# Performance work log

Hardware: AMD Instinct MI355X
Metric: run time of the kernel (lower is better)

The kernel has to match this reference:

```python
import jax, jax.numpy as jnp
import numpy as np

B, C, H, W = 16, 256, 56, 56
G, K, R = 16, 3, 2
CR = C // R          # reduced channels = 128
KKG = K * K * G      # span output channels = 144
EPS = 1e-5


def setup_inputs() -> dict:
    key = jax.random.key(0)
    ks = jax.random.split(key, 5)
    return {
        "x": jax.random.normal(ks[0], (B, C, H, W), jnp.float32),
        "w_reduce": jax.random.normal(ks[1], (CR, C), jnp.float32) * 0.05,
        "b_reduce": jax.random.normal(ks[2], (CR,), jnp.float32) * 0.05,
        "gamma": jnp.ones((CR,), jnp.float32),
        "beta": jnp.zeros((CR,), jnp.float32),
        "w_span": jax.random.normal(ks[3], (KKG, CR), jnp.float32) * 0.05,
        "b_span": jax.random.normal(ks[4], (KKG,), jnp.float32) * 0.05,
    }


def _conv1x1(x, w, bias):
    # 1x1 conv == channel contraction
    return jnp.einsum('bchw,oc->bohw', x, w) + bias[None, :, None, None]


def _involution(x, w_reduce, b_reduce, gamma, beta, w_span, b_span):
    b, c, h, w = x.shape
    # kernel-generation branch: reduce -> BN (batch stats) -> ReLU -> span
    t = _conv1x1(x, w_reduce, b_reduce)
    mu = t.mean(axis=(0, 2, 3), keepdims=True)
    var = t.var(axis=(0, 2, 3), keepdims=True)  # biased, as torch BN training
    t = (t - mu) * jax.lax.rsqrt(var + EPS)
    t = t * gamma[None, :, None, None] + beta[None, :, None, None]
    t = jax.nn.relu(t)
    kern = _conv1x1(t, w_span, b_span)  # [b, k*k*g, h, w]
    # 'b (k j g) h w -> b g (k j) h w'
    kern = kern.reshape(b, K, K, G, h, w).transpose(0, 3, 1, 2, 4, 5)
    kern = kern.reshape(b, G, K * K, h, w)
    # unfold x into [b, g, d, k*k, h, w] via shifted padded slices (no dense im2col buffer write pattern beyond necessity)
    p = K // 2
    xp = jnp.pad(x, ((0, 0), (0, 0), (p, p), (p, p)))
    patches = jnp.stack(
        [xp[:, :, i:i + h, j:j + w] for i in range(K) for j in range(K)],
        axis=2)  # [b, c, k*k, h, w]
    patches = patches.reshape(b, G, c // G, K * K, h, w)
    out = jnp.einsum('bgdxhw,bgxhw->bgdhw', patches, kern)  # weighted window sum
    return out.reshape(b, c, h, w)


def reference(x, w_reduce, b_reduce, gamma, beta, w_span, b_span):
    return _involution(x, w_reduce, b_reduce, gamma, beta, w_span, b_span)
```

## Files before the change

### kernel.cpp

```cpp
#include <hip/hip_runtime.h>
#include <hip/hip_bf16.h>

#define B_   16
#define C_   256
#define HW_  3136
#define W_   56
#define CR_  128
#define KKG_ 144
#define G_   16
#define NPOS (B_*HW_)
#define EPS_ 1e-5f
#define NBLK1 1568
#define NBLK3 784

typedef float f32x4 __attribute__((ext_vector_type(4)));
typedef short s16x8 __attribute__((ext_vector_type(8)));
typedef short s16x4 __attribute__((ext_vector_type(4)));

#define T2_OFF_B    0
#define KERN_OFF_B  12845056
#define GACC_OFF_B  27295744
#define WBFR_OFF_B  27296768
#define WBFS_OFF_B  27362304

__device__ inline unsigned short f2bf(float f) {
    unsigned u = __float_as_uint(f);
    u += 0x7fff + ((u >> 16) & 1);
    return (unsigned short)(u >> 16);
}
__device__ inline float bf2f(unsigned short h) {
    return __uint_as_float(((unsigned)h) << 16);
}
__device__ inline unsigned pkcvt(float a, float b) {
    float2 f2; f2.x = a; f2.y = b;
    __hip_bfloat162 h = __float22bfloat162_rn(f2);
    union { __hip_bfloat162 h2; unsigned u; } cv; cv.h2 = h;
    return cv.u;
}

typedef const __attribute__((address_space(1))) unsigned int* gas_t;
typedef __attribute__((address_space(3))) unsigned int* las_t;
__device__ inline void gload_lds16(const void* g, void* l) {
    __builtin_amdgcn_global_load_lds((gas_t)g, (las_t)l, 16, 0, 0);
}
__device__ inline void barrier_raw() {
    __builtin_amdgcn_sched_barrier(0);
    __builtin_amdgcn_s_barrier();
    __builtin_amdgcn_sched_barrier(0);
}

__global__ __launch_bounds__(256) void prep_cast(
    const float* __restrict__ w_reduce, const float* __restrict__ w_span,
    unsigned short* __restrict__ wbfr, unsigned short* __restrict__ wbfs,
    float* __restrict__ gacc)
{
    int idx = blockIdx.x * 256 + threadIdx.x;
    if (idx < 256) gacc[idx] = 0.0f;
    if (idx < 32768) {
        wbfr[idx] = f2bf(w_reduce[idx]);
    } else {
        int k = idx - 32768;
        if (k < 18432) wbfs[k] = f2bf(w_span[k]);
    }
}

__global__ __launch_bounds__(256, 4) void reduce_mfma(
    const float* __restrict__ x, const unsigned short* __restrict__ wbfr,
    unsigned short* __restrict__ t2, float* __restrict__ gacc)
{
    __shared__ __align__(16) float xb3[3][1024];
    __shared__ __align__(16) short awb[3][4096];
    __shared__ float redp[128][2], redq[128][2];

    const int tid = threadIdx.x;
    const int lane = tid & 63, wv = tid >> 6;
    const int q = lane >> 4, i = lane & 15;
    const int q8 = q * 8;
    const int mrow = (wv & 1) * 64;
    const int pw = (wv >> 1) * 16;
    const int blk = blockIdx.x;
    const int b = blk / 98;
    const int p0 = (blk % 98) * 32;

    const int c_st = tid >> 3;
    const int swz = ((tid & 7) ^ ((c_st >> 1) & 7)) * 4;
    const float* xlane = x + (size_t)b * C_ * HW_ + (size_t)c_st * HW_ + p0 + swz;
    const unsigned short* wA0 = wbfr + (size_t)(tid >> 2) * C_ + (tid & 3) * 8;
    const unsigned short* wA1 = wA0 + (size_t)64 * C_;
    const int wvu4 = (tid & ~63) * 4;
    const int wvu8 = (tid & ~63) * 8;

    #define STAGE1(ch, bi) do {                                          \
        gload_lds16(xlane + (size_t)(ch) * 32 * HW_, &xb3[bi][wvu4]);    \
        gload_lds16(wA0 + (ch) * 32, &awb[bi][wvu8]);                    \
        gload_lds16(wA1 + (ch) * 32, &awb[bi][2048 + wvu8]);             \
    } while (0)

    const int p_loc = pw + i;
    const int pg = p_loc >> 2, pe = p_loc & 3;

    f32x4 acc[4] = {};

    STAGE1(0, 0);
    STAGE1(1, 1);

    #pragma unroll
    for (int ch = 0; ch < 8; ch++) {
        const int cur = ch % 3;
        if (ch < 7) asm volatile("s_waitcnt vmcnt(3)" ::: "memory");
        else        asm volatile("s_waitcnt vmcnt(0)" ::: "memory");
        barrier_raw();
        if (ch == 0) STAGE1(2, 2);
        if (ch == 1) STAGE1(3, 0);
        if (ch == 2) STAGE1(4, 1);
        if (ch == 3) STAGE1(5, 2);
        if (ch == 4) STAGE1(6, 0);
        if (ch == 5) STAGE1(7, 1);

        s16x8 af[4];
        #pragma unroll
        for (int mt = 0; mt < 4; mt++)
            af[mt] = *(const s16x8*)&awb[cur][(mrow + mt * 16 + i) * 32 + q8];
        float f[8];
        #pragma unroll
        for (int k = 0; k < 8; k++) {
            int cl = q8 + k;
            int slot = pg ^ ((cl >> 1) & 7);
            f[k] = xb3[cur][cl * 32 + slot * 4 + pe];
        }
        union { s16x8 v; unsigned u[4]; } Bv;
        #pragma unroll
        for (int k2 = 0; k2 < 4; k2++) Bv.u[k2] = pkcvt(f[2*k2], f[2*k2+1]);

        #pragma unroll
        for (int mt = 0; mt < 4; mt++)
            acc[mt] = __builtin_amdgcn_mfma_f32_16x16x32_bf16(
                af[mt], Bv.v, acc[mt], 0, 0, 0);
    }
    #undef STAGE1

    const int p = p0 + pw + i;
    #pragma unroll
    for (int mt = 0; mt < 4; mt++) {
        uint2 pr;
        pr.x = pkcvt(acc[mt][0], acc[mt][1]);
        pr.y = pkcvt(acc[mt][2], acc[mt][3]);
        *(uint2*)(t2 + ((size_t)b * HW_ + p) * CR_ + mrow + mt * 16 + q * 4) = pr;
        #pragma unroll
        for (int reg = 0; reg < 4; reg++) {
            float v = acc[mt][reg];
            float s = v, ss = v * v;
            #pragma unroll
            for (int m = 1; m < 16; m <<= 1) {
                s  += __shfl_xor(s, m);
                ss += __shfl_xor(ss, m);
            }
            if (i == 0) {
                int o = mrow + mt * 16 + q * 4 + reg;
                redp[o][wv >> 1] = s;
                redq[o][wv >> 1] = ss;
            }
        }
    }
    __syncthreads();
    if (tid < 128) atomicAdd(&gacc[tid], redp[tid][0] + redp[tid][1]);
    else           atomicAdd(&gacc[tid], redq[tid - 128][0] + redq[tid - 128][1]);
}

__global__ __launch_bounds__(256, 3) void span_mfma(
    const unsigned short* __restrict__ t2, const unsigned short* __restrict__ wbfs,
    const float* __restrict__ b_span, const float* __restrict__ gacc,
    const float* __restrict__ gamma, const float* __restrict__ beta,
    unsigned short* __restrict__ kern)
{
    __shared__ __align__(16) short aw[144 * 128];
    __shared__ __align__(16) short bb3[3][2048];
    __shared__ float scs[128], shs[128], bsp[144];

    const int tid = threadIdx.x;
    const int lane = tid & 63, wv = tid >> 6;
    const int q = lane >> 4, i = lane & 15;
    const int q8 = q * 8;
    const int blk = blockIdx.x;
    const int b = blk / 49;
    const int p0 = (blk % 49) * 64;

    if (tid < 128) {
        float s = gacc[tid], ss = gacc[128 + tid];
        const float inv_n = 1.0f / (float)NPOS;
        float mu = s * inv_n;
        float var = ss * inv_n - mu * mu;
        float sc = gamma[tid] * rsqrtf(var + EPS_);
        scs[tid] = sc;
        shs[tid] = beta[tid] - mu * sc;
    }
    if (tid < 144) bsp[tid] = b_span[tid];
    __syncthreads();

    const unsigned short* tlane =
        t2 + ((size_t)b * HW_ + p0 + (tid >> 2)) * CR_ + (tid & 3) * 8;
    const int wvu8 = (tid & ~63) * 8;

    #pragma unroll
    for (int e = 0; e < 9; e++) {
        int U = tid + e * 256;
        int r = U >> 4, u = U & 15;
        gload_lds16(wbfs + (size_t)r * CR_ + ((u ^ (r & 7)) * 8),
                    &aw[((tid & ~63) + e * 256) * 8]);
    }
    gload_lds16(tlane,      &bb3[0][wvu8]);
    gload_lds16(tlane + 32, &bb3[1][wvu8]);

    f32x4 acc[9] = {};

    #pragma unroll
    for (int ch = 0; ch < 4; ch++) {
        const int cur = ch % 3;
        if (ch < 3) asm volatile("s_waitcnt vmcnt(1)" ::: "memory");
        else        asm volatile("s_waitcnt vmcnt(0)" ::: "memory");
        barrier_raw();
        if (ch == 0) gload_lds16(tlane + 64, &bb3[2][wvu8]);
        if (ch == 1) gload_lds16(tlane + 96, &bb3[0][wvu8]);

        s16x8 raw = *(const s16x8*)&bb3[cur][(wv * 16 + i) * 32 + q8];
        const int cb = ch * 32 + q8;
        float f[8];
        #pragma unroll
        for (int k = 0; k < 8; k++)
            f[k] = fmaxf(fmaf(bf2f((unsigned short)raw[k]),
                              scs[cb + k], shs[cb + k]), 0.0f);
        union { s16x8 v; unsigned u[4]; } Bv;
        #pragma unroll
        for (int k2 = 0; k2 < 4; k2++) Bv.u[k2] = pkcvt(f[2*k2], f[2*k2+1]);

        #pragma unroll
        for (int mt = 0; mt < 9; mt++) {
            int r = mt * 16 + i;
            int slot = (ch * 4 + q) ^ (r & 7);
            s16x8 af = *(const s16x8*)&aw[r * 128 + slot * 8];
            acc[mt] = __builtin_amdgcn_mfma_f32_16x16x32_bf16(
                af, Bv.v, acc[mt], 0, 0, 0);
        }
    }

    const int p = p0 + wv * 16 + i;
    #pragma unroll
    for (int mt = 0; mt < 9; mt++) {
        #pragma unroll
        for (int reg = 0; reg < 4; reg++) {
            int o2 = mt * 16 + q * 4 + reg;
            int row = (o2 & 15) * 9 + (o2 >> 4);
            kern[((size_t)b * KKG_ + row) * HW_ + p] = f2bf(acc[mt][reg] + bsp[o2]);
        }
    }
}

__global__ __launch_bounds__(256) void involution_apply(
    const float* __restrict__ x, const unsigned short* __restrict__ kern,
    float* __restrict__ out)
{
    const int gtid = blockIdx.x * 256 + threadIdx.x;
    const int pu  = gtid % 784;
    const int bg  = gtid / 784;
    const int g = bg & 15;
    const int b = bg >> 4;
    const int pix0 = pu * 4;
    const int h = pix0 / W_;
    const int w0 = pix0 % W_;

    const unsigned short* kb = kern + ((size_t)(b * G_ + g) * 9) * HW_ + pix0;
    float kvf[9][4];
    #pragma unroll
    for (int kk = 0; kk < 9; kk++) {
        s16x4 kraw = *(const s16x4*)(kb + (size_t)kk * HW_);
        #pragma unroll
        for (int j = 0; j < 4; j++)
            kvf[kk][j] = bf2f((unsigned short)kraw[j]);
    }

    const float* xg = x + (size_t)(b * C_ + g * 16) * HW_;
    float* og = out + (size_t)(b * C_ + g * 16) * HW_ + pix0;

    const bool has_l = (w0 > 0);
    const bool has_r = (w0 + 4 < W_);
    const int loff = has_l ? (w0 - 1) : w0;
    const int roff = has_r ? (w0 + 4) : w0;

    #pragma unroll
    for (int d = 0; d < 16; d++) {
        f32x4 acc = {0.0f, 0.0f, 0.0f, 0.0f};
        const float* xd = xg + (size_t)d * HW_;
        #pragma unroll
        for (int di = 0; di < 3; di++) {
            const int hh = h + di - 1;
            if (hh < 0 || hh >= W_) continue;
            const float* xr = xd + hh * W_;
            float4 mid = *(const float4*)(xr + w0);
            float lv = xr[loff];
            float rv = xr[roff];
            float win[6];
            win[0] = has_l ? lv : 0.0f;
            win[1] = mid.x; win[2] = mid.y; win[3] = mid.z; win[4] = mid.w;
            win[5] = has_r ? rv : 0.0f;
            #pragma unroll
            for (int dj = 0; dj < 3; dj++) {
                #pragma unroll
                for (int j = 0; j < 4; j++)
                    acc[j] = fmaf(win[dj + j], kvf[di * 3 + dj][j], acc[j]);
            }
        }
        *(f32x4*)(og + (size_t)d * HW_) = acc;
    }
}

extern "C" void kernel_launch(void* const* d_in, const int* in_sizes, int n_in,
                              void* d_out, int out_size, void* d_ws, size_t ws_size,
                              hipStream_t stream) {
    const float* x        = (const float*)d_in[0];
    const float* w_reduce = (const float*)d_in[1];
    const float* gamma    = (const float*)d_in[3];
    const float* beta     = (const float*)d_in[4];
    const float* w_span   = (const float*)d_in[5];
    const float* b_span   = (const float*)d_in[6];
    float* out = (float*)d_out;

    char* wsb = (char*)d_ws;
    unsigned short* t2   = (unsigned short*)(wsb + T2_OFF_B);
    unsigned short* kern = (unsigned short*)(wsb + KERN_OFF_B);
    float*          gacc = (float*)(wsb + GACC_OFF_B);
    unsigned short* wbfr = (unsigned short*)(wsb + WBFR_OFF_B);
    unsigned short* wbfs = (unsigned short*)(wsb + WBFS_OFF_B);

    prep_cast<<<200, 256, 0, stream>>>(w_reduce, w_span, wbfr, wbfs, gacc);
    reduce_mfma<<<NBLK1, 256, 0, stream>>>(x, wbfr, t2, gacc);
    span_mfma<<<NBLK3, 256, 0, stream>>>(t2, wbfs, b_span, gacc, gamma, beta, kern);
    involution_apply<<<(B_ * G_ * HW_ / 4) / 256, 256, 0, stream>>>(x, kern, out);
}
```

Measured before the change: 198.8 us.

## Double reduce-kernel position tile and replace BN atomics with per-block partials

The reduce GEMM kernel now handles 64 positions per block instead of 32, halving the grid to 784 blocks. Each wave computes two N-tiles, so each A-fragment load is reused twice, and the x staging buffer doubles with an adjusted swizzle. The BN sum and sum-of-squares atomics are replaced by per-block partial writes. A new bn_finalize kernel reduces those partials and produces scale and shift, which removes atomic contention but adds one kernel launch. Occupancy drops from 4 to 3 blocks per CU because of the larger shared memory footprint.

```diff
diff --git a/kernel.cpp b/kernel.cpp
--- a/kernel.cpp
+++ b/kernel.cpp
@@ -10,8 +10,7 @@
 #define G_   16
 #define NPOS (B_*HW_)
 #define EPS_ 1e-5f
-#define NBLK1 1568
-#define NBLK3 784
+#define NBLK 784
 
 typedef float f32x4 __attribute__((ext_vector_type(4)));
 typedef short s16x8 __attribute__((ext_vector_type(8)));
@@ -19,9 +18,10 @@
 
 #define T2_OFF_B    0
 #define KERN_OFF_B  12845056
-#define GACC_OFF_B  27295744
-#define WBFR_OFF_B  27296768
-#define WBFS_OFF_B  27362304
+#define GP_OFF_B    27295744
+#define STAT_OFF_B  28098560
+#define WBFR_OFF_B  28099584
+#define WBFS_OFF_B  28165120
 
 __device__ inline unsigned short f2bf(float f) {
     unsigned u = __float_as_uint(f);
@@ -51,11 +51,9 @@
 
 __global__ __launch_bounds__(256) void prep_cast(
     const float* __restrict__ w_reduce, const float* __restrict__ w_span,
-    unsigned short* __restrict__ wbfr, unsigned short* __restrict__ wbfs,
-    float* __restrict__ gacc)
+    unsigned short* __restrict__ wbfr, unsigned short* __restrict__ wbfs)
 {
     int idx = blockIdx.x * 256 + threadIdx.x;
-    if (idx < 256) gacc[idx] = 0.0f;
     if (idx < 32768) {
         wbfr[idx] = f2bf(w_reduce[idx]);
     } else {
@@ -64,11 +62,11 @@
     }
 }
 
-__global__ __launch_bounds__(256, 4) void reduce_mfma(
+__global__ __launch_bounds__(256, 3) void reduce_mfma(
     const float* __restrict__ x, const unsigned short* __restrict__ wbfr,
-    unsigned short* __restrict__ t2, float* __restrict__ gacc)
-{
-    __shared__ __align__(16) float xb3[3][1024];
+    unsigned short* __restrict__ t2, float* __restrict__ gp)
+{
+    __shared__ __align__(16) float xb3[3][2048];
     __shared__ __align__(16) short awb[3][4096];
     __shared__ float redp[128][2], redq[128][2];
 
@@ -77,29 +75,30 @@
     const int q = lane >> 4, i = lane & 15;
     const int q8 = q * 8;
     const int mrow = (wv & 1) * 64;
-    const int pw = (wv >> 1) * 16;
+    const int pw = (wv >> 1) * 32;
     const int blk = blockIdx.x;
-    const int b = blk / 98;
-    const int p0 = (blk % 98) * 32;
-
-    const int c_st = tid >> 3;
-    const int swz = ((tid & 7) ^ ((c_st >> 1) & 7)) * 4;
-    const float* xlane = x + (size_t)b * C_ * HW_ + (size_t)c_st * HW_ + p0 + swz;
+    const int b = blk / 49;
+    const int p0 = (blk % 49) * 64;
+
+    const int ce0 = tid >> 4, slot = tid & 15;
+    const int ce1 = ce0 + 16;
+    const float* xs0 = x + (size_t)b * C_ * HW_ + (size_t)ce0 * HW_ + p0
+                         + ((slot ^ ((ce0 >> 2) & 7)) << 2);
+    const float* xs1 = x + (size_t)b * C_ * HW_ + (size_t)ce1 * HW_ + p0
+                         + ((slot ^ ((ce1 >> 2) & 7)) << 2);
     const unsigned short* wA0 = wbfr + (size_t)(tid >> 2) * C_ + (tid & 3) * 8;
     const unsigned short* wA1 = wA0 + (size_t)64 * C_;
     const int wvu4 = (tid & ~63) * 4;
     const int wvu8 = (tid & ~63) * 8;
 
-    #define STAGE1(ch, bi) do {                                          \
-        gload_lds16(xlane + (size_t)(ch) * 32 * HW_, &xb3[bi][wvu4]);    \
-        gload_lds16(wA0 + (ch) * 32, &awb[bi][wvu8]);                    \
-        gload_lds16(wA1 + (ch) * 32, &awb[bi][2048 + wvu8]);             \
+    #define STAGE1(ch, bi) do {                                            \
+        gload_lds16(xs0 + (size_t)(ch) * 32 * HW_, &xb3[bi][wvu4]);        \
+        gload_lds16(xs1 + (size_t)(ch) * 32 * HW_, &xb3[bi][1024 + wvu4]); \
+        gload_lds16(wA0 + (ch) * 32, &awb[bi][wvu8]);                      \
+        gload_lds16(wA1 + (ch) * 32, &awb[bi][2048 + wvu8]);               \
     } while (0)
 
-    const int p_loc = pw + i;
-    const int pg = p_loc >> 2, pe = p_loc & 3;
-
-    f32x4 acc[4] = {};
+    f32x4 acc[4][2] = {};
 
     STAGE1(0, 0);
     STAGE1(1, 1);
@@ -107,7 +106,7 @@
     #pragma unroll
     for (int ch = 0; ch < 8; ch++) {
         const int cur = ch % 3;
-        if (ch < 7) asm volatile("s_waitcnt vmcnt(3)" ::: "memory");
+        if (ch < 7) asm volatile("s_waitcnt vmcnt(4)" ::: "memory");
         else        asm volatile("s_waitcnt vmcnt(0)" ::: "memory");
         barrier_raw();
         if (ch == 0) STAGE1(2, 2);
@@ -121,35 +120,48 @@
         #pragma unroll
         for (int mt = 0; mt < 4; mt++)
             af[mt] = *(const s16x8*)&awb[cur][(mrow + mt * 16 + i) * 32 + q8];
-        float f[8];
-        #pragma unroll
-        for (int k = 0; k < 8; k++) {
-            int cl = q8 + k;
-            int slot = pg ^ ((cl >> 1) & 7);
-            f[k] = xb3[cur][cl * 32 + slot * 4 + pe];
-        }
-        union { s16x8 v; unsigned u[4]; } Bv;
-        #pragma unroll
-        for (int k2 = 0; k2 < 4; k2++) Bv.u[k2] = pkcvt(f[2*k2], f[2*k2+1]);
+
+        s16x8 bfr[2];
+        #pragma unroll
+        for (int nt = 0; nt < 2; nt++) {
+            const int p_loc = pw + nt * 16 + i;
+            const int pg = p_loc >> 2, pe = p_loc & 3;
+            float f[8];
+            #pragma unroll
+            for (int k = 0; k < 8; k++) {
+                int cl = q8 + k;
+                f[k] = xb3[cur][cl * 64 + ((pg ^ ((cl >> 2) & 7)) << 2) + pe];
+            }
+            union { s16x8 v; unsigned u[4]; } Bv;
+            #pragma unroll
+            for (int k2 = 0; k2 < 4; k2++) Bv.u[k2] = pkcvt(f[2*k2], f[2*k2+1]);
+            bfr[nt] = Bv.v;
+        }
 
         #pragma unroll
         for (int mt = 0; mt < 4; mt++)
-            acc[mt] = __builtin_amdgcn_mfma_f32_16x16x32_bf16(
-                af[mt], Bv.v, acc[mt], 0, 0, 0);
+            #pragma unroll
+            for (int nt = 0; nt < 2; nt++)
+                acc[mt][nt] = __builtin_amdgcn_mfma_f32_16x16x32_bf16(
+                    af[mt], bfr[nt], acc[mt][nt], 0, 0, 0);
     }
     #undef STAGE1
 
-    const int p = p0 + pw + i;
     #pragma unroll
     for (int mt = 0; mt < 4; mt++) {
-        uint2 pr;
-        pr.x = pkcvt(acc[mt][0], acc[mt][1]);
-        pr.y = pkcvt(acc[mt][2], acc[mt][3]);
-        *(uint2*)(t2 + ((size_t)b * HW_ + p) * CR_ + mrow + mt * 16 + q * 4) = pr;
+        #pragma unroll
+        for (int nt = 0; nt < 2; nt++) {
+            int p = p0 + pw + nt * 16 + i;
+            uint2 pr;
+            pr.x = pkcvt(acc[mt][nt][0], acc[mt][nt][1]);
+            pr.y = pkcvt(acc[mt][nt][2], acc[mt][nt][3]);
+            *(uint2*)(t2 + ((size_t)b * HW_ + p) * CR_ + mrow + mt * 16 + q * 4) = pr;
+        }
         #pragma unroll
         for (int reg = 0; reg < 4; reg++) {
-            float v = acc[mt][reg];
-            float s = v, ss = v * v;
+            float v0 = acc[mt][0][reg], v1 = acc[mt][1][reg];
+            float s = v0 + v1;
+            float ss = v0 * v0 + v1 * v1;
             #pragma unroll
             for (int m = 1; m < 16; m <<= 1) {
                 s  += __shfl_xor(s, m);
@@ -163,14 +175,46 @@
         }
     }
     __syncthreads();
-    if (tid < 128) atomicAdd(&gacc[tid], redp[tid][0] + redp[tid][1]);
-    else           atomicAdd(&gacc[tid], redq[tid - 128][0] + redq[tid - 128][1]);
+    if (tid < 128)
+        gp[(size_t)tid * NBLK + blk] = redp[tid][0] + redp[tid][1];
+    else
+        gp[(size_t)tid * NBLK + blk] = redq[tid - 128][0] + redq[tid - 128][1];
+}
+
+__global__ __launch_bounds__(256) void bn_finalize(
+    const float* __restrict__ gp, const float* __restrict__ gamma,
+    const float* __restrict__ beta, float* __restrict__ stats)
+{
+    const int o = blockIdx.x;
+    const int tid = threadIdx.x;
+    float s = 0.f, ss = 0.f;
+    for (int idx = tid; idx < NBLK; idx += 256) {
+        s  += gp[(size_t)o * NBLK + idx];
+        ss += gp[(size_t)(128 + o) * NBLK + idx];
+    }
+    #pragma unroll
+    for (int m = 1; m < 64; m <<= 1) {
+        s  += __shfl_xor(s, m);
+        ss += __shfl_xor(ss, m);
+    }
+    __shared__ float rs[4], rss[4];
+    if ((tid & 63) == 0) { rs[tid >> 6] = s; rss[tid >> 6] = ss; }
+    __syncthreads();
+    if (tid == 0) {
+        s  = rs[0] + rs[1] + rs[2] + rs[3];
+        ss = rss[0] + rss[1] + rss[2] + rss[3];
+        float inv_n = 1.0f / (float)NPOS;
+        float mu = s * inv_n;
+        float var = ss * inv_n - mu * mu;
+        float sc = gamma[o] * rsqrtf(var + EPS_);
+        stats[o] = sc;
+        stats[128 + o] = beta[o] - mu * sc;
+    }
 }
 
 __global__ __launch_bounds__(256, 3) void span_mfma(
     const unsigned short* __restrict__ t2, const unsigned short* __restrict__ wbfs,
-    const float* __restrict__ b_span, const float* __restrict__ gacc,
-    const float* __restrict__ gamma, const float* __restrict__ beta,
+    const float* __restrict__ b_span, const float* __restrict__ stats,
     unsigned short* __restrict__ kern)
 {
     __shared__ __align__(16) short aw[144 * 128];
@@ -185,15 +229,7 @@
     const int b = blk / 49;
     const int p0 = (blk % 49) * 64;
 
-    if (tid < 128) {
-        float s = gacc[tid], ss = gacc[128 + tid];
-        const float inv_n = 1.0f / (float)NPOS;
-        float mu = s * inv_n;
-        float var = ss * inv_n - mu * mu;
-        float sc = gamma[tid] * rsqrtf(var + EPS_);
-        scs[tid] = sc;
-        shs[tid] = beta[tid] - mu * sc;
-    }
+    if (tid < 128) { scs[tid] = stats[tid]; shs[tid] = stats[128 + tid]; }
     if (tid < 144) bsp[tid] = b_span[tid];
     __syncthreads();
 
@@ -327,12 +363,14 @@
     char* wsb = (char*)d_ws;
     unsigned short* t2   = (unsigned short*)(wsb + T2_OFF_B);
     unsigned short* kern = (unsigned short*)(wsb + KERN_OFF_B);
-    float*          gacc = (float*)(wsb + GACC_OFF_B);
+    float*          gp    = (float*)(wsb + GP_OFF_B);
+    float*          stats = (float*)(wsb + STAT_OFF_B);
     unsigned short* wbfr = (unsigned short*)(wsb + WBFR_OFF_B);
     unsigned short* wbfs = (unsigned short*)(wsb + WBFS_OFF_B);
 
-    prep_cast<<<200, 256, 0, stream>>>(w_reduce, w_span, wbfr, wbfs, gacc);
-    reduce_mfma<<<NBLK1, 256, 0, stream>>>(x, wbfr, t2, gacc);
-    span_mfma<<<NBLK3, 256, 0, stream>>>(t2, wbfs, b_span, gacc, gamma, beta, kern);
+    prep_cast<<<200, 256, 0, stream>>>(w_reduce, w_span, wbfr, wbfs);
+    reduce_mfma<<<NBLK, 256, 0, stream>>>(x, wbfr, t2, gp);
+    bn_finalize<<<128, 256, 0, stream>>>(gp, gamma, beta, stats);
+    span_mfma<<<NBLK, 256, 0, stream>>>(t2, wbfs, b_span, stats, kern);
     involution_apply<<<(B_ * G_ * HW_ / 4) / 256, 256, 0, stream>>>(x, kern, out);
 }
```

After: 170.0 us. -14.5%, faster.
